# Performance work log

Measured on AMD Instinct MI355X. Metric: run time of the kernel, lower is better.

## Reference

```python
import jax, jax.numpy as jnp
import numpy as np

B, NV, NF, E = 8, 2048, 4096, 12288
DIM, DCE, DCB, K = 512, 64, 192, 128
NQ, BITS, GROUPS = 2, 14, 8


def _conv1d(x, w, b):
    # x [B, C, N], w [O, I, 3]
    y = jax.lax.conv_general_dilated(x, w, (1,), [(1, 1)], dimension_numbers=('NCH', 'OIH', 'NCH'))
    return y + b[None, :, None]


def _group_norm(x, g, b, groups=GROUPS, eps=1e-5):
    B_, C, N = x.shape
    xg = x.reshape(B_, groups, C // groups, N)
    mu = xg.mean(axis=(2, 3), keepdims=True)
    var = xg.var(axis=(2, 3), keepdims=True)
    xn = ((xg - mu) * jax.lax.rsqrt(var + eps)).reshape(B_, C, N)
    return xn * g[None, :, None] + b[None, :, None]


def _block(x, w, bias, g, beta, m):
    x = x * m
    x = _conv1d(x, w, bias)
    x = x * m
    x = _group_norm(x, g, beta)
    return jax.nn.silu(x)


def _forward(vertices, coor_embed, W_in, b_in, sage_Wl, sage_Wr, sage_b, W_cb, b_cb,
             lfq_in, lfq_out, W_out, b_out, dec_conv_w, dec_conv_b, dec_gn_g, dec_gn_b,
             W_logits, b_logits, faces, face_edges, face_edges_mask, face_mask):
    lo, hi = -1.0, 1.0
    # discretize_coors
    disc = jnp.clip(jnp.round((vertices - lo) / (hi - lo) * K - 0.5), 0, K - 1).astype(jnp.int32)
    # gather per-face vertex coords: [b, nf, 3, 3] -> [b, nf, 9]
    fc = jax.vmap(lambda v, f: v[f])(disc, faces).reshape(B, NF, 9)
    emb = coor_embed[fc].reshape(B, NF, 9 * DCE)
    x = (emb @ W_in + b_in).reshape(B * NF, DIM)
    N = B * NF
    x = jnp.concatenate([x, jnp.zeros((1, DIM), x.dtype)], axis=0)  # pad node
    offset = (jnp.arange(B) * NF)[:, None, None]
    edges = jnp.where(face_edges_mask[:, None, :], face_edges + offset, N)
    edges = edges.transpose(1, 0, 2).reshape(2, -1)
    src, tgt = edges[0], edges[1]
    ones = jnp.ones(src.shape, x.dtype)
    for l in range(sage_Wl.shape[0]):  # SAGEConv, mean aggregation
        s = jax.ops.segment_sum(x[src], tgt, num_segments=N + 1)
        c = jax.ops.segment_sum(ones, tgt, num_segments=N + 1)
        x = (s / jnp.clip(c, 1.0)[:, None]) @ sage_Wl[l] + x @ sage_Wr[l] + sage_b[l]
    x = x[:-1].reshape(B, NF, DIM)
    # quantize path: scatter-mean face-corner embeddings onto vertices
    fe = (x @ W_cb + b_cb).reshape(B, NF * 3, DCB)
    faces_m = jnp.where(face_mask[:, :, None], faces, NV).reshape(B, NF * 3).astype(jnp.int32)
    num = jax.vmap(lambda e, i: jax.ops.segment_sum(e, i, num_segments=NV + 1))(fe, faces_m)
    den = jax.vmap(lambda i: jax.ops.segment_sum(jnp.ones((NF * 3,), fe.dtype), i, num_segments=NV + 1))(faces_m)
    avg = num / jnp.clip(den, 1e-5)[..., None]
    # residual lookup-free quantization with straight-through
    res, quant = avg, jnp.zeros_like(avg)
    for q in range(NQ):
        h = res @ lfq_in[q]
        bits = jnp.where(h > 0, 1.0, -1.0).astype(h.dtype)
        bits = h + jax.lax.stop_gradient(bits - h)
        outq = bits @ lfq_out[q]
        quant = quant + outq
        res = res - outq
    # gather quantized vertex codes back to faces
    feo = jax.vmap(lambda qv, i: qv[i])(quant, faces_m).reshape(B, NF, 3 * DCB)
    feo = feo @ W_out + b_out
    # conv resnet decoder
    xd = feo.transpose(0, 2, 1)  # [b, dim, nf]
    m = face_mask[:, None, :].astype(xd.dtype)
    for blk in range(dec_conv_w.shape[0]):
        h0 = xd
        for sub in range(2):
            h0 = _block(h0, dec_conv_w[blk, sub], dec_conv_b[blk, sub], dec_gn_g[blk, sub], dec_gn_b[blk, sub], m)
        xd = h0 + xd
    dec = xd.transpose(0, 2, 1)
    return (dec @ W_logits + b_logits).reshape(B, NF, 9, K)


def setup_inputs():
    key = jax.random.key(0)
    ks = jax.random.split(key, 24)
    r = lambda i, shape, s=0.02: jax.random.normal(ks[i], shape, jnp.float32) * s
    return dict(
        vertices=jax.random.uniform(ks[0], (B, NV, 3), jnp.float32, -0.95, 0.95),
        faces=jax.random.randint(ks[1], (B, NF, 3), 0, NV),
        face_edges=jax.random.randint(ks[2], (B, 2, E), 0, NF),
        face_edges_mask=jnp.ones((B, E), bool),
        face_mask=jnp.ones((B, NF), bool),
        coor_embed=r(3, (K, DCE), 1.0),
        W_in=r(4, (9 * DCE, DIM)), b_in=r(5, (DIM,)),
        sage_Wl=r(6, (2, DIM, DIM)), sage_Wr=r(7, (2, DIM, DIM)), sage_b=r(8, (2, DIM)),
        W_cb=r(9, (DIM, 3 * DCB)), b_cb=r(10, (3 * DCB,)),
        lfq_in=r(11, (NQ, DCB, BITS), 0.05), lfq_out=r(12, (NQ, BITS, DCB), 0.05),
        W_out=r(13, (3 * DCB, DIM)), b_out=r(14, (DIM,)),
        dec_conv_w=r(15, (2, 2, DIM, DIM, 3)), dec_conv_b=r(16, (2, 2, DIM)),
        dec_gn_g=jnp.ones((2, 2, DIM), jnp.float32), dec_gn_b=jnp.zeros((2, 2, DIM), jnp.float32),
        W_logits=r(17, (DIM, 9 * K)), b_logits=r(18, (9 * K,)),
    )


def reference(vertices, faces, face_edges, face_edges_mask, face_mask, coor_embed, W_in, b_in,
              sage_Wl, sage_Wr, sage_b, W_cb, b_cb, lfq_in, lfq_out, W_out, b_out,
              dec_conv_w, dec_conv_b, dec_gn_g, dec_gn_b, W_logits, b_logits):
    return _forward(vertices, coor_embed, W_in, b_in, sage_Wl, sage_Wr, sage_b, W_cb, b_cb,
                    lfq_in, lfq_out, W_out, b_out, dec_conv_w, dec_conv_b, dec_gn_g, dec_gn_b,
                    W_logits, b_logits, faces, face_edges, face_edges_mask, face_mask)
```

## Files before the change

kernel.cpp:

```cpp
#include <hip/hip_runtime.h>
#include <hip/hip_bf16.h>
#include <cstdint>
#include <cstddef>

constexpr int BB    = 8;
constexpr int NV    = 2048;
constexpr int NF    = 4096;
constexpr int NE    = 12288;
constexpr int DIM   = 512;
constexpr int DCB   = 192;
constexpr int NQv   = 2;
constexpr int BITSv = 14;
constexpr int NFACE = BB * NF;
constexpr int NEDGE = BB * NE;
constexpr int NVB   = BB * NV;
constexpr int NFP   = NF + 2;

typedef __attribute__((ext_vector_type(8))) short bf16x8;
typedef __attribute__((ext_vector_type(4))) float f32x4;

static __device__ __forceinline__ float b2f(unsigned short u) {
    union { unsigned u; float f; } x; x.u = ((unsigned)u) << 16; return x.f;
}
static __device__ __forceinline__ unsigned short f2bu(float v) {
    __hip_bfloat16 h = __float2bfloat16(v);
    return __builtin_bit_cast(unsigned short, h);
}
static __device__ __forceinline__ void split3(float v, unsigned short& a, unsigned short& b,
                                              unsigned short& c) {
    a = f2bu(v);            float r  = v - b2f(a);
    b = f2bu(r);            float r2 = r - b2f(b);
    c = f2bu(r2);
}
static __device__ __forceinline__ void load16(const void* g, void* l) {
    __builtin_amdgcn_global_load_lds((const __attribute__((address_space(1))) unsigned int*)g,
                                     (__attribute__((address_space(3))) unsigned int*)l, 16, 0, 0);
}

static __device__ __forceinline__ void xcd_swizzle(int& bx, int& by)
{
    const int nx  = (int)gridDim.x;
    const int lin = (int)(blockIdx.x + gridDim.x * blockIdx.y);
    const int xcd = lin & 7;
    const int j   = lin >> 3;
    bx = j % nx;
    by = xcd * 32 + j / nx;
}

__global__ void k_codes(const float* __restrict__ vertices, const int* __restrict__ faces,
                        int* __restrict__ fc)
{
    const int idx = blockIdx.x * 256 + threadIdx.x;
    if (idx >= NFACE * 9) return;
    const int r = idx / 9, p = idx - r * 9;
    const int i = p / 3, j = p - i * 3;
    const int b = r >> 12;
    const int v = faces[r * 3 + i];
    const float coord = vertices[((size_t)b * NV + v) * 3 + j];
    float t = rintf((coord + 1.0f) * 0.5f * 128.0f - 0.5f);
    t = fminf(fmaxf(t, 0.0f), 127.0f);
    fc[r * 12 + p] = (int)t;
}

__global__ __launch_bounds__(256)
void k_build_T(const float* __restrict__ ce, const float* __restrict__ W_in, float* __restrict__ T)
{
    const int p = blockIdx.x;
    const int c = blockIdx.y;
    const int o = threadIdx.x * 2;
    float s0 = 0.f, s1 = 0.f;
    for (int d = 0; d < 64; ++d) {
        const float e = ce[c * 64 + d];
        const float* wr_ = W_in + (size_t)(p * 64 + d) * 512 + o;
        s0 = fmaf(e, wr_[0], s0);
        s1 = fmaf(e, wr_[1], s1);
    }
    float* dst = T + ((size_t)p * 128 + c) * 512 + o;
    dst[0] = s0; dst[1] = s1;
}

__global__ __launch_bounds__(256)
void k_xin(const int* __restrict__ fc, const float* __restrict__ T,
           const float* __restrict__ b_in,
           unsigned short* __restrict__ x0, unsigned short* __restrict__ x1,
           unsigned short* __restrict__ x2)
{
    const int r = blockIdx.x;
    const int o = threadIdx.x * 2;
    float s0 = b_in[o], s1 = b_in[o + 1];
#pragma unroll
    for (int p = 0; p < 9; ++p) {
        const int c = fc[r * 12 + p];
        const float* t = T + ((size_t)p * 128 + c) * 512 + o;
        s0 += t[0]; s1 += t[1];
    }
    unsigned short h0, m0, l0, h1, m1, l1;
    split3(s0, h0, m0, l0); split3(s1, h1, m1, l1);
    const size_t ob = (size_t)r * 512 + o;
    ushort2 u;
    u.x = h0; u.y = h1; *(ushort2*)&x0[ob] = u;
    u.x = m0; u.y = m1; *(ushort2*)&x1[ob] = u;
    u.x = l0; u.y = l1; *(ushort2*)&x2[ob] = u;
}

__global__ void k_count_e(const int* __restrict__ fe, int* __restrict__ deg)
{
    const int e = blockIdx.x * 256 + threadIdx.x;
    if (e >= NEDGE) return;
    const int b = e / NE, ee = e - b * NE;
    atomicAdd(&deg[fe[(b * 2 + 1) * NE + ee] + b * NF], 1);
}
__global__ void k_fill_e(const int* __restrict__ fe, int* __restrict__ cursor, int* __restrict__ srcE)
{
    const int e = blockIdx.x * 256 + threadIdx.x;
    if (e >= NEDGE) return;
    const int b = e / NE, ee = e - b * NE;
    const int src = fe[(b * 2 + 0) * NE + ee] + b * NF;
    const int tgt = fe[(b * 2 + 1) * NE + ee] + b * NF;
    srcE[atomicAdd(&cursor[tgt], 1)] = src;
}
__global__ void k_count_v(const int* __restrict__ faces, int* __restrict__ deg)
{
    const int q = blockIdx.x * 256 + threadIdx.x;
    if (q >= NEDGE) return;
    atomicAdd(&deg[(q / (NF * 3)) * NV + faces[q]], 1);
}
__global__ void k_fill_v(const int* __restrict__ faces, int* __restrict__ cursor, int* __restrict__ cid)
{
    const int q = blockIdx.x * 256 + threadIdx.x;
    if (q >= NEDGE) return;
    const int b = q / (NF * 3);
    cid[atomicAdd(&cursor[b * NV + faces[q]], 1)] = q;
}
__global__ void k_scan(const int* __restrict__ deg, int* __restrict__ rowstart,
                       int* __restrict__ cursor, int n)
{
    __shared__ int part[256];
    const int t = threadIdx.x;
    const int chunk = n / 256;
    int s = 0;
    for (int i = 0; i < chunk; ++i) s += deg[t * chunk + i];
    part[t] = s;
    __syncthreads();
    for (int o = 1; o < 256; o <<= 1) {
        int v = (t >= o) ? part[t - o] : 0;
        __syncthreads();
        part[t] += v;
        __syncthreads();
    }
    int base = (t == 0) ? 0 : part[t - 1];
    for (int i = 0; i < chunk; ++i) {
        const int idx = t * chunk + i;
        const int d = deg[idx];
        rowstart[idx] = base;
        cursor[idx]   = base;
        base += d;
    }
    if (t == 255) rowstart[n] = base;
}

__global__ void k_agg_e3(const unsigned short* __restrict__ p0, const unsigned short* __restrict__ p1,
                         const unsigned short* __restrict__ p2, const int* __restrict__ rowstart,
                         const int* __restrict__ srcE,
                         unsigned short* __restrict__ o0, unsigned short* __restrict__ o1,
                         unsigned short* __restrict__ o2)
{
    const int t = threadIdx.x;
    const int r = blockIdx.x * 2 + (t >> 7);
    const int c4 = (t & 127) << 2;
    const int s = rowstart[r], e = rowstart[r + 1];
    float a0 = 0.f, a1 = 0.f, a2 = 0.f, a3 = 0.f;
    for (int i = s; i < e; ++i) {
        const size_t ba = (size_t)srcE[i] * 512 + c4;
        const ushort4 u0 = *(const ushort4*)(p0 + ba);
        const ushort4 u1 = *(const ushort4*)(p1 + ba);
        const ushort4 u2 = *(const ushort4*)(p2 + ba);
        a0 += b2f(u0.x) + b2f(u1.x) + b2f(u2.x);
        a1 += b2f(u0.y) + b2f(u1.y) + b2f(u2.y);
        a2 += b2f(u0.z) + b2f(u1.z) + b2f(u2.z);
        a3 += b2f(u0.w) + b2f(u1.w) + b2f(u2.w);
    }
    const float inv = 1.0f / fmaxf((float)(e - s), 1.0f);
    a0 *= inv; a1 *= inv; a2 *= inv; a3 *= inv;
    ushort4 q0, q1, q2;
    split3(a0, q0.x, q1.x, q2.x); split3(a1, q0.y, q1.y, q2.y);
    split3(a2, q0.z, q1.z, q2.z); split3(a3, q0.w, q1.w, q2.w);
    const size_t ob = (size_t)r * 512 + c4;
    *(ushort4*)(o0 + ob) = q0; *(ushort4*)(o1 + ob) = q1; *(ushort4*)(o2 + ob) = q2;
}

__global__ void k_agg_verts(const float* __restrict__ fe, const int* __restrict__ rowstart,
                            const int* __restrict__ cid, float* __restrict__ avg)
{
    const int r = blockIdx.x;
    const int c = threadIdx.x;
    const int s = rowstart[r], e = rowstart[r + 1];
    float a = 0.f;
    for (int i = s; i < e; ++i) {
        const int q = cid[i];
        const int face = q / 3, corner = q - face * 3;
        a += fe[(size_t)face * 576 + corner * 192 + c];
    }
    avg[(size_t)r * 192 + c] = a / fmaxf((float)(e - s), 1e-5f);
}

__global__ void k_lfq(const float* __restrict__ avg, const float* __restrict__ lfq_in,
                      const float* __restrict__ lfq_out, float* __restrict__ quant)
{
    __shared__ float res[DCB];
    __shared__ float qacc[DCB];
    __shared__ float bits[BITSv];
    const int r = blockIdx.x;
    const int t = threadIdx.x;
    for (int c = t; c < DCB; c += 64) {
        res[c]  = avg[(size_t)r * DCB + c];
        qacc[c] = 0.f;
    }
    __syncthreads();
    for (int q = 0; q < NQv; ++q) {
        if (t < BITSv) {
            float h = 0.f;
            const float* w = lfq_in + q * DCB * BITSv + t;
            for (int k = 0; k < DCB; ++k) h += res[k] * w[k * BITSv];
            bits[t] = (h > 0.f) ? 1.f : -1.f;
        }
        __syncthreads();
        for (int c = t; c < DCB; c += 64) {
            float o = 0.f;
            const float* w2 = lfq_out + q * BITSv * DCB + c;
#pragma unroll
            for (int j = 0; j < BITSv; ++j) o += bits[j] * w2[j * DCB];
            qacc[c] += o;
            res[c]  -= o;
        }
        __syncthreads();
    }
    for (int c = t; c < DCB; c += 64) quant[(size_t)r * DCB + c] = qacc[c];
}

__global__ void k_gather_feo(const float* __restrict__ quant, const int* __restrict__ faces,
                             unsigned short* __restrict__ feo)
{
    const long long idx = (long long)blockIdx.x * 256 + threadIdx.x;
    if (idx >= (long long)NFACE * 576) return;
    const int row = (int)(idx / 576);
    const int col = (int)(idx - (long long)row * 576);
    const int i = col / 192, c = col - i * 192;
    const int b = row >> 12;
    const int v = faces[row * 3 + i];
    feo[idx] = f2bu(quant[((size_t)b * NV + v) * 192 + c]);
}

__global__ void k_pack_plain(const float* __restrict__ src, unsigned short* __restrict__ dst,
                             int Kd, int Nd)
{
    const int idx = blockIdx.x * 256 + threadIdx.x;
    if (idx >= Kd * Nd) return;
    const int n = idx / Kd, k = idx - n * Kd;
    dst[idx] = f2bu(src[(size_t)k * Nd + n]);
}
__global__ void k_pack_conv(const float* __restrict__ w, unsigned short* __restrict__ bt)
{
    const int idx = blockIdx.x * 256 + threadIdx.x;
    if (idx >= 4 * 512 * 1536) return;
    const int ws_ = idx / (512 * 1536);
    const int rem = idx - ws_ * 512 * 1536;
    const int o = rem / 1536, k = rem - o * 1536;
    const int tap = k >> 9, i = k & 511;
    bt[idx] = f2bu(w[(((size_t)(ws_ * 512 + o)) * 512 + i) * 3 + tap]);
}
static __device__ __forceinline__ unsigned short bplane(float w, int inner)
{
    unsigned short w0, w1, w2; split3(w, w0, w1, w2);
    const int bsel = (inner == 3) ? 2 : ((inner == 1 || inner == 4) ? 1 : 0);
    return (bsel == 0) ? w0 : ((bsel == 1) ? w1 : w2);
}
__global__ void k_pack_sage3(const float* __restrict__ wl, const float* __restrict__ wr,
                             unsigned short* __restrict__ bt)
{
    const int idx = blockIdx.x * 256 + threadIdx.x;
    if (idx >= 2 * 512 * 6144) return;
    const int l = idx / (512 * 6144);
    const int rem = idx - l * 512 * 6144;
    const int n = rem / 6144, k = rem - n * 6144;
    const int seg = k >> 9, kk = k & 511;
    const int inner = (seg >= 6) ? seg - 6 : seg;
    const float* W = ((seg >= 6) ? wr : wl) + (size_t)l * 512 * 512;
    bt[idx] = bplane(W[kk * 512 + n], inner);
}
__global__ void k_pack_cb3(const float* __restrict__ w, unsigned short* __restrict__ bt)
{
    const int idx = blockIdx.x * 256 + threadIdx.x;
    if (idx >= 640 * 3072) return;
    const int n = idx / 3072, k = idx - n * 3072;
    const int seg = k >> 9, kk = k & 511;
    const float v = (n < 576) ? w[kk * 576 + n] : 0.f;
    bt[idx] = bplane(v, seg);
}

__global__ void k_zero_guards(unsigned short* __restrict__ xdp, unsigned short* __restrict__ hp)
{
    const int idx = blockIdx.x * 256 + threadIdx.x;
    if (idx >= 8192) return;
    const int b = idx >> 10, rem = idx & 1023;
    const int row = (rem >> 9) ? (NF + 1) : 0;
    const int c = rem & 511;
    const size_t o = ((size_t)b * NFP + row) * 512 + c;
    xdp[o] = 0; hp[o] = 0;
}

template <int NSEG, int OUTE>
__global__ __launch_bounds__(256)
void k_mm_enc(const unsigned short* __restrict__ g0, const unsigned short* __restrict__ g1,
              const unsigned short* __restrict__ g2, const unsigned short* __restrict__ xA0,
              const unsigned short* __restrict__ xA1, const unsigned short* __restrict__ xA2,
              const unsigned short* __restrict__ Bt, const float* __restrict__ bias,
              void* __restrict__ C0, void* __restrict__ C1, void* __restrict__ C2, int N)
{
    constexpr int K = NSEG * 512;
    constexpr int NGRP = (NSEG == 12) ? 6 : 3;
    __shared__ __align__(16) short As[128 * 32];
    __shared__ __align__(16) short Bs[3][128 * 32];

    int bx, by;
    xcd_swizzle(bx, by);
    const int t  = threadIdx.x;
    const int m0 = by * 128;
    const int n0 = bx * 128;
    const int w  = t >> 6, l = t & 63;
    const int wr = w >> 1, wc = w & 1;
    const int lr = l & 15, lq = l >> 4;

    f32x4 acc[4][4];
#pragma unroll
    for (int i = 0; i < 4; ++i)
#pragma unroll
        for (int j = 0; j < 4; ++j)
#pragma unroll
            for (int r = 0; r < 4; ++r) acc[i][j][r] = 0.f;

    const unsigned short* const APL[6] = {g0, g1, g2, xA0, xA1, xA2};
    constexpr int SB[7]  = {0, 3, 5, 6, 9, 11, 12};
    constexpr int SL[12] = {0, 1, 3, 2, 4, 5, 6, 7, 9, 8, 10, 11};

#pragma unroll 1
    for (int kk = 0; kk < 512; kk += 32) {
#pragma unroll
        for (int grp = 0; grp < NGRP; ++grp) {
            const unsigned short* Ab = APL[grp];
            const int ns = SB[grp + 1] - SB[grp];
#pragma unroll
            for (int half = 0; half < 2; ++half) {
                const int ch = (half << 8) + t;
                const int row = ch >> 2, kq = ch & 3;
                load16(Ab + (size_t)(m0 + row) * 512 + kk + kq * 8, &As[ch * 8]);
#pragma unroll
                for (int s = 0; s < 3; ++s) {
                    if (s < ns) {
                        const int seg = SL[SB[grp] + s];
                        load16(Bt + (size_t)(n0 + row) * K + seg * 512 + kk + kq * 8,
                               &Bs[s][ch * 8]);
                    }
                }
            }
            __syncthreads();
            bf16x8 aF[4];
#pragma unroll
            for (int i = 0; i < 4; ++i)
                aF[i] = *(const bf16x8*)&As[(wr * 64 + i * 16 + lr) * 32 + lq * 8];
#pragma unroll
            for (int s = 0; s < 3; ++s) {
                if (s < ns) {
                    bf16x8 bF[4];
#pragma unroll
                    for (int j = 0; j < 4; ++j)
                        bF[j] = *(const bf16x8*)&Bs[s][(wc * 64 + j * 16 + lr) * 32 + lq * 8];
#pragma unroll
                    for (int i = 0; i < 4; ++i)
#pragma unroll
                        for (int j = 0; j < 4; ++j)
                            acc[i][j] = __builtin_amdgcn_mfma_f32_16x16x32_bf16(aF[i], bF[j],
                                                                                acc[i][j], 0, 0, 0);
                }
            }
            __syncthreads();
        }
    }

#pragma unroll
    for (int i = 0; i < 4; ++i) {
#pragma unroll
        for (int r = 0; r < 4; ++r) {
            const int m = m0 + wr * 64 + i * 16 + lq * 4 + r;
#pragma unroll
            for (int j = 0; j < 4; ++j) {
                const int n = n0 + wc * 64 + j * 16 + lr;
                if (OUTE == 0) {
                    const float v = acc[i][j][r] + bias[n];
                    unsigned short u0, u1, u2; split3(v, u0, u1, u2);
                    const size_t ob = (size_t)m * 512 + n;
                    ((unsigned short*)C0)[ob] = u0;
                    ((unsigned short*)C1)[ob] = u1;
                    ((unsigned short*)C2)[ob] = u2;
                } else {
                    if (n < N) ((float*)C0)[(size_t)m * N + n] = acc[i][j][r] + bias[n];
                }
            }
        }
    }
}

template <int AMODE, int OUT>
__global__ __launch_bounds__(256)
void k_mm(const unsigned short* __restrict__ a0, const unsigned short* __restrict__ Bt,
          const float* __restrict__ bias, void* __restrict__ C0, int N, int K)
{
    __shared__ __align__(16) short As[128 * 32];
    __shared__ __align__(16) short Bs[128 * 32];

    int bx, by;
    xcd_swizzle(bx, by);
    const int t  = threadIdx.x;
    const int m0 = by * 128;
    const int n0 = bx * 128;
    const int w  = t >> 6, l = t & 63;
    const int wr = w >> 1, wc = w & 1;
    const int lr = l & 15, lq = l >> 4;

    f32x4 acc[4][4];
#pragma unroll
    for (int i = 0; i < 4; ++i)
#pragma unroll
        for (int j = 0; j < 4; ++j)
#pragma unroll
            for (int r = 0; r < 4; ++r) acc[i][j][r] = 0.f;

    for (int k0 = 0; k0 < K; k0 += 32) {
#pragma unroll
        for (int half = 0; half < 2; ++half) {
            const int ch = (half << 8) + t;
            const int row = ch >> 2, kq = ch & 3;
            const int m = m0 + row;
            const unsigned short* ga;
            if (AMODE == 0) {
                ga = a0 + (size_t)m * K + k0 + kq * 8;
            } else if (AMODE == 1) {
                ga = a0 + (((size_t)(m + ((m >> 12) << 1) + 1)) << 9) + k0 + kq * 8;
            } else {
                const int tap = k0 >> 9;
                ga = a0 + (((size_t)(m + ((m >> 12) << 1) + tap)) << 9) + (k0 & 511) + kq * 8;
            }
            load16(ga, &As[ch * 8]);
            load16(Bt + (size_t)(n0 + row) * K + k0 + kq * 8, &Bs[ch * 8]);
        }
        __syncthreads();

        bf16x8 aF[4], bF[4];
#pragma unroll
        for (int i = 0; i < 4; ++i) {
            aF[i] = *(const bf16x8*)&As[(wr * 64 + i * 16 + lr) * 32 + lq * 8];
            bF[i] = *(const bf16x8*)&Bs[(wc * 64 + i * 16 + lr) * 32 + lq * 8];
        }
#pragma unroll
        for (int i = 0; i < 4; ++i)
#pragma unroll
            for (int j = 0; j < 4; ++j)
                acc[i][j] = __builtin_amdgcn_mfma_f32_16x16x32_bf16(aF[i], bF[j], acc[i][j], 0, 0, 0);
        __syncthreads();
    }

#pragma unroll
    for (int i = 0; i < 4; ++i) {
#pragma unroll
        for (int r = 0; r < 4; ++r) {
            const int m = m0 + wr * 64 + i * 16 + lq * 4 + r;
#pragma unroll
            for (int j = 0; j < 4; ++j) {
                const int n = n0 + wc * 64 + j * 16 + lr;
                const float bv = (OUT == 1) ? ((n < N) ? bias[n] : 0.f) : bias[n];
                const float v = acc[i][j][r] + bv;
                if (OUT == 0) {
                    ((unsigned short*)C0)[(size_t)m * 512 + n] = f2bu(v);
                } else if (OUT == 1) {
                    if (n < N) ((float*)C0)[(size_t)m * N + n] = v;
                } else {
                    ((unsigned short*)C0)[((size_t)(m + ((m >> 12) << 1) + 1)) * 512 + n] = f2bu(v);
                }
            }
        }
    }
}

__global__ __launch_bounds__(256)
void k_mm_conv(const unsigned short* __restrict__ ap, const unsigned short* __restrict__ Bt,
               const float* __restrict__ bias, unsigned short* __restrict__ C0)
{
    __shared__ __align__(16) short As[132 * 32];
    __shared__ __align__(16) short Bs[3][128 * 32];

    int bx, by;
    xcd_swizzle(bx, by);
    const int t  = threadIdx.x;
    const int m0 = by * 128;
    const int n0 = bx * 128;
    const int w  = t >> 6, l = t & 63;
    const int wr = w >> 1, wc = w & 1;
    const int lr = l & 15, lq = l >> 4;
    const int pbase = m0 + ((m0 >> 12) << 1);

    f32x4 acc[4][4];
#pragma unroll
    for (int i = 0; i < 4; ++i)
#pragma unroll
        for (int j = 0; j < 4; ++j)
#pragma unroll
            for (int r = 0; r < 4; ++r) acc[i][j][r] = 0.f;

#pragma unroll 1
    for (int kk = 0; kk < 512; kk += 32) {
#pragma unroll
        for (int rnd = 0; rnd < 2; ++rnd) {
            const int ch = (rnd << 8) + t;
            const int row = ch >> 2, kq = ch & 3;
            load16(ap + (((size_t)(pbase + row)) << 9) + kk + kq * 8, &As[ch * 8]);
        }
        if (t < 8) {
            const int ch = 512 + t;
            const int row = ch >> 2, kq = ch & 3;
            load16(ap + (((size_t)(pbase + row)) << 9) + kk + kq * 8, &As[ch * 8]);
        }
#pragma unroll
        for (int tap = 0; tap < 3; ++tap) {
#pragma unroll
            for (int half = 0; half < 2; ++half) {
                const int ch = (half << 8) + t;
                const int row = ch >> 2, kq = ch & 3;
                load16(Bt + (size_t)(n0 + row) * 1536 + tap * 512 + kk + kq * 8, &Bs[tap][ch * 8]);
            }
        }
        __syncthreads();
#pragma unroll
        for (int tap = 0; tap < 3; ++tap) {
            bf16x8 aF[4], bF[4];
#pragma unroll
            for (int i = 0; i < 4; ++i) {
                aF[i] = *(const bf16x8*)&As[(tap + wr * 64 + i * 16 + lr) * 32 + lq * 8];
                bF[i] = *(const bf16x8*)&Bs[tap][(wc * 64 + i * 16 + lr) * 32 + lq * 8];
            }
#pragma unroll
            for (int i = 0; i < 4; ++i)
#pragma unroll
                for (int j = 0; j < 4; ++j)
                    acc[i][j] = __builtin_amdgcn_mfma_f32_16x16x32_bf16(aF[i], bF[j], acc[i][j], 0, 0, 0);
        }
        __syncthreads();
    }

#pragma unroll
    for (int i = 0; i < 4; ++i) {
#pragma unroll
        for (int r = 0; r < 4; ++r) {
            const int m = m0 + wr * 64 + i * 16 + lq * 4 + r;
#pragma unroll
            for (int j = 0; j < 4; ++j) {
                const int n = n0 + wc * 64 + j * 16 + lr;
                C0[(size_t)m * 512 + n] = f2bu(acc[i][j][r] + bias[n]);
            }
        }
    }
}

__global__ __launch_bounds__(256)
void k_gn_stats(const unsigned short* __restrict__ h, float* __restrict__ stats)
{
    const int bg = blockIdx.x;
    const int b = bg >> 3, g = bg & 7;
    const int t = threadIdx.x;
    float sum = 0.f, sq = 0.f;
    const unsigned short* base = h + (size_t)b * NF * 512 + g * 64;
    for (int n = t; n < NF; n += 256) {
        const unsigned short* p = base + (size_t)n * 512;
#pragma unroll
        for (int c = 0; c < 64; c += 4) {
            const ushort4 v4 = *(const ushort4*)(p + c);
            const float f0 = b2f(v4.x), f1 = b2f(v4.y), f2 = b2f(v4.z), f3 = b2f(v4.w);
            sum += f0 + f1 + f2 + f3;
            sq  += f0 * f0 + f1 * f1 + f2 * f2 + f3 * f3;
        }
    }
    __shared__ float s1[256], s2[256];
    s1[t] = sum; s2[t] = sq;
    __syncthreads();
    for (int o = 128; o > 0; o >>= 1) {
        if (t < o) { s1[t] += s1[t + o]; s2[t] += s2[t + o]; }
        __syncthreads();
    }
    if (t == 0) {
        const float cntf = (float)(NF * 64);
        const float mean = s1[0] / cntf;
        const float var  = s2[0] / cntf - mean * mean;
        stats[bg * 2 + 0] = mean;
        stats[bg * 2 + 1] = rsqrtf(var + 1e-5f);
    }
}

__global__ void k_gn_apply(const unsigned short* __restrict__ h, const float* __restrict__ stats,
                           const float* __restrict__ gamma, const float* __restrict__ beta,
                           const unsigned short* __restrict__ resid_pad, unsigned short* __restrict__ dst_pad)
{
    const int idx = blockIdx.x * 256 + threadIdx.x;
    if (idx >= NFACE * 512 / 4) return;
    const int i4 = idx * 4;
    const int c = i4 & 511;
    const int row = i4 >> 9;
    const int b = row >> 12;
    const int g = c >> 6;
    const float mean = stats[(b * 8 + g) * 2 + 0];
    const float rstd = stats[(b * 8 + g) * 2 + 1];
    const ushort4 v4 = *(const ushort4*)(h + (size_t)row * 512 + c);
    const float4 gm = *(const float4*)&gamma[c];
    const float4 bt = *(const float4*)&beta[c];
    float o0 = (b2f(v4.x) - mean) * rstd * gm.x + bt.x;
    float o1 = (b2f(v4.y) - mean) * rstd * gm.y + bt.y;
    float o2 = (b2f(v4.z) - mean) * rstd * gm.z + bt.z;
    float o3 = (b2f(v4.w) - mean) * rstd * gm.w + bt.w;
    o0 = o0 / (1.f + expf(-o0));
    o1 = o1 / (1.f + expf(-o1));
    o2 = o2 / (1.f + expf(-o2));
    o3 = o3 / (1.f + expf(-o3));
    const size_t po = ((size_t)row + (size_t)(row >> 12) * 2 + 1) * 512 + c;
    if (resid_pad) {
        const ushort4 r4 = *(const ushort4*)(resid_pad + po);
        o0 += b2f(r4.x); o1 += b2f(r4.y); o2 += b2f(r4.z); o3 += b2f(r4.w);
    }
    ushort4 o;
    o.x = f2bu(o0); o.y = f2bu(o1); o.z = f2bu(o2); o.w = f2bu(o3);
    *(ushort4*)(dst_pad + po) = o;
}

extern "C" void kernel_launch(void* const* d_in, const int* in_sizes, int n_in,
                              void* d_out, int out_size, void* d_ws, size_t ws_size,
                              hipStream_t stream)
{
    const float* vertices   = (const float*)d_in[0];
    const int*   faces      = (const int*)  d_in[1];
    const int*   face_edges = (const int*)  d_in[2];
    const float* coor_embed = (const float*)d_in[5];
    const float* W_in    = (const float*)d_in[6];
    const float* b_in    = (const float*)d_in[7];
    const float* sage_Wl = (const float*)d_in[8];
    const float* sage_Wr = (const float*)d_in[9];
    const float* sage_b  = (const float*)d_in[10];
    const float* W_cb    = (const float*)d_in[11];
    const float* b_cb    = (const float*)d_in[12];
    const float* lfq_in  = (const float*)d_in[13];
    const float* lfq_out = (const float*)d_in[14];
    const float* W_out   = (const float*)d_in[15];
    const float* b_out   = (const float*)d_in[16];
    const float* dconv_w = (const float*)d_in[17];
    const float* dconv_b = (const float*)d_in[18];
    const float* dgn_g   = (const float*)d_in[19];
    const float* dgn_b   = (const float*)d_in[20];
    const float* W_log   = (const float*)d_in[21];
    const float* b_log   = (const float*)d_in[22];

    char* base = (char*)d_ws;
    size_t off = 0;
    auto alloc = [&](size_t bytes) { char* p = base + off; off += (bytes + 255) & ~(size_t)255; return p; };

    const size_t PLANE  = (size_t)NFACE * 512 * 2;
    char* P1 = alloc(3 * PLANE);
    char* P2 = alloc(3 * PLANE);
    char* P3 = alloc(3 * PLANE + 65536);

    unsigned short* x0 = (unsigned short*)P1;
    unsigned short* x1 = x0 + (size_t)NFACE * 512;
    unsigned short* x2 = x1 + (size_t)NFACE * 512;
    unsigned short* g0 = (unsigned short*)P2;
    unsigned short* g1 = g0 + (size_t)NFACE * 512;
    unsigned short* g2 = g1 + (size_t)NFACE * 512;
    unsigned short* y0 = (unsigned short*)P3;
    unsigned short* y1 = y0 + (size_t)NFACE * 512;
    unsigned short* y2 = y1 + (size_t)NFACE * 512;
    float*          fe   = (float*)P3;
    unsigned short* feo  = (unsigned short*)P2;
    float*          avg  = (float*)(P2 + (size_t)40 * 1024 * 1024);
    float*          quant = avg + (size_t)NVB * 192;
    unsigned short* xdp  = (unsigned short*)P3;
    unsigned short* hp   = xdp + (size_t)BB * NFP * 512;
    unsigned short* cbuf = hp + (size_t)BB * NFP * 512;

    int*   fc = (int*)  alloc((size_t)NFACE * 12 * 4);
    float* T  = (float*)alloc((size_t)9 * 128 * 512 * 4);
    unsigned short* bt_sage = (unsigned short*)alloc(2ull * 512 * 6144 * 2);
    unsigned short* bt_cb   = (unsigned short*)alloc(640ull * 3072 * 2);
    unsigned short* bt_out  = (unsigned short*)alloc(512ull * 576 * 2);
    unsigned short* bt_log  = (unsigned short*)alloc(1152ull * 512 * 2);
    unsigned short* bt_conv = (unsigned short*)alloc(4ull * 512 * 1536 * 2);
    int* degE = (int*)alloc(32768 * 4);
    int* rsE  = (int*)alloc(32772 * 4);
    int* curE = (int*)alloc(32768 * 4);
    int* srcE = (int*)alloc(98304 * 4);
    int* degV = (int*)alloc(16384 * 4);
    int* rsV  = (int*)alloc(16388 * 4);
    int* curV = (int*)alloc(16384 * 4);
    int* cidV = (int*)alloc(98304 * 4);
    float* stats = (float*)alloc(128 * 4);

    const dim3 blk(256);

    k_pack_sage3<<<dim3(24576), blk, 0, stream>>>(sage_Wl, sage_Wr, bt_sage);
    k_pack_cb3  <<<dim3(7680),  blk, 0, stream>>>(W_cb, bt_cb);
    k_pack_plain<<<dim3(1152),  blk, 0, stream>>>(W_out, bt_out, 576, 512);
    k_pack_plain<<<dim3(2304),  blk, 0, stream>>>(W_log, bt_log, 512, 1152);
    k_pack_conv <<<dim3(12288), blk, 0, stream>>>(dconv_w, bt_conv);

    hipMemsetAsync(degE, 0, 32768 * 4, stream);
    hipMemsetAsync(degV, 0, 16384 * 4, stream);
    k_count_e<<<dim3(384), blk, 0, stream>>>(face_edges, degE);
    k_count_v<<<dim3(384), blk, 0, stream>>>(faces, degV);
    k_scan<<<dim3(1), blk, 0, stream>>>(degE, rsE, curE, 32768);
    k_scan<<<dim3(1), blk, 0, stream>>>(degV, rsV, curV, 16384);
    k_fill_e<<<dim3(384), blk, 0, stream>>>(face_edges, curE, srcE);
    k_fill_v<<<dim3(384), blk, 0, stream>>>(faces, curV, cidV);

    k_codes<<<dim3(1152), blk, 0, stream>>>(vertices, faces, fc);
    k_build_T<<<dim3(9, 128), blk, 0, stream>>>(coor_embed, W_in, T);
    k_xin<<<dim3(NFACE), blk, 0, stream>>>(fc, T, b_in, x0, x1, x2);

    k_agg_e3<<<dim3(16384), blk, 0, stream>>>(x0, x1, x2, rsE, srcE, g0, g1, g2);
    k_mm_enc<12, 0><<<dim3(4, 256), blk, 0, stream>>>(g0, g1, g2, x0, x1, x2,
        bt_sage, sage_b, y0, y1, y2, 512);

    k_agg_e3<<<dim3(16384), blk, 0, stream>>>(y0, y1, y2, rsE, srcE, g0, g1, g2);
    k_mm_enc<12, 0><<<dim3(4, 256), blk, 0, stream>>>(g0, g1, g2, y0, y1, y2,
        bt_sage + (size_t)512 * 6144, sage_b + 512, x0, x1, x2, 512);

    k_mm_enc<6, 1><<<dim3(5, 256), blk, 0, stream>>>(x0, x1, x2, nullptr, nullptr, nullptr,
        bt_cb, b_cb, fe, nullptr, nullptr, 576);

    k_agg_verts<<<dim3(NVB), dim3(192), 0, stream>>>(fe, rsV, cidV, avg);
    k_lfq<<<dim3(NVB), dim3(64), 0, stream>>>(avg, lfq_in, lfq_out, quant);
    k_gather_feo<<<dim3(73728), blk, 0, stream>>>(quant, faces, feo);

    k_zero_guards<<<dim3(32), blk, 0, stream>>>(xdp, hp);
    k_mm<0, 2><<<dim3(4, 256), blk, 0, stream>>>(feo, bt_out, b_out, xdp, 512, 576);

    for (int blkI = 0; blkI < 2; ++blkI) {
        k_mm_conv<<<dim3(4, 256), blk, 0, stream>>>(xdp,
            bt_conv + (size_t)(blkI * 2 + 0) * 512 * 1536, dconv_b + (blkI * 2 + 0) * 512, cbuf);
        k_gn_stats<<<dim3(64), blk, 0, stream>>>(cbuf, stats);
        k_gn_apply<<<dim3(16384), blk, 0, stream>>>(cbuf, stats,
            dgn_g + (blkI * 2 + 0) * 512, dgn_b + (blkI * 2 + 0) * 512, nullptr, hp);
        k_mm_conv<<<dim3(4, 256), blk, 0, stream>>>(hp,
            bt_conv + (size_t)(blkI * 2 + 1) * 512 * 1536, dconv_b + (blkI * 2 + 1) * 512, cbuf);
        k_gn_stats<<<dim3(64), blk, 0, stream>>>(cbuf, stats);
        k_gn_apply<<<dim3(16384), blk, 0, stream>>>(cbuf, stats,
            dgn_g + (blkI * 2 + 1) * 512, dgn_b + (blkI * 2 + 1) * 512, xdp, xdp);
    }

    k_mm<1, 1><<<dim3(9, 256), blk, 0, stream>>>(xdp, bt_log, b_log, (float*)d_out, 1152, 512);
}
```

Measured before the change: 1.838 ms.

## Fuse face gather into output GEMM and GroupNorm stats into conv epilogue

Replaces the per-element face-corner gather kernel with a small bf16 cast of the vertex quant table, and a new GEMM kernel that gathers A rows through face indices staged in shared memory. This removes the materialized 576-wide feo buffer. The separate GroupNorm statistics kernel is removed: the conv GEMM epilogue reduces sum and sum-of-squares per block and atomically adds them into zeroed stats buffers, one per conv, and mean/rstd are computed in the apply kernel. The weight pack kernels now compute split3 once per weight and write all planes. The trade-off is float atomics, which make the order nondeterministic, and a one-pass E[x²]-mean² variance that is less numerically stable.

Result: faster. 1.754 ms (-4.5%).

```diff
diff --git a/kernel.cpp b/kernel.cpp
--- a/kernel.cpp
+++ b/kernel.cpp
@@ -238,17 +238,14 @@
     for (int c = t; c < DCB; c += 64) quant[(size_t)r * DCB + c] = qacc[c];
 }
 
-__global__ void k_gather_feo(const float* __restrict__ quant, const int* __restrict__ faces,
-                             unsigned short* __restrict__ feo)
-{
-    const long long idx = (long long)blockIdx.x * 256 + threadIdx.x;
-    if (idx >= (long long)NFACE * 576) return;
-    const int row = (int)(idx / 576);
-    const int col = (int)(idx - (long long)row * 576);
-    const int i = col / 192, c = col - i * 192;
-    const int b = row >> 12;
-    const int v = faces[row * 3 + i];
-    feo[idx] = f2bu(quant[((size_t)b * NV + v) * 192 + c]);
+__global__ void k_quant_cast(const float* __restrict__ q, unsigned short* __restrict__ qb)
+{
+    const int idx = blockIdx.x * 256 + threadIdx.x;
+    if (idx >= NVB * 48) return;
+    const float4 v = *(const float4*)(q + (size_t)idx * 4);
+    ushort4 o;
+    o.x = f2bu(v.x); o.y = f2bu(v.y); o.z = f2bu(v.z); o.w = f2bu(v.w);
+    *(ushort4*)(qb + (size_t)idx * 4) = o;
 }
 
 __global__ void k_pack_plain(const float* __restrict__ src, unsigned short* __restrict__ dst,
@@ -269,33 +266,35 @@
     const int tap = k >> 9, i = k & 511;
     bt[idx] = f2bu(w[(((size_t)(ws_ * 512 + o)) * 512 + i) * 3 + tap]);
 }
-static __device__ __forceinline__ unsigned short bplane(float w, int inner)
-{
-    unsigned short w0, w1, w2; split3(w, w0, w1, w2);
-    const int bsel = (inner == 3) ? 2 : ((inner == 1 || inner == 4) ? 1 : 0);
-    return (bsel == 0) ? w0 : ((bsel == 1) ? w1 : w2);
-}
 __global__ void k_pack_sage3(const float* __restrict__ wl, const float* __restrict__ wr,
                              unsigned short* __restrict__ bt)
 {
     const int idx = blockIdx.x * 256 + threadIdx.x;
-    if (idx >= 2 * 512 * 6144) return;
-    const int l = idx / (512 * 6144);
-    const int rem = idx - l * 512 * 6144;
-    const int n = rem / 6144, k = rem - n * 6144;
-    const int seg = k >> 9, kk = k & 511;
-    const int inner = (seg >= 6) ? seg - 6 : seg;
-    const float* W = ((seg >= 6) ? wr : wl) + (size_t)l * 512 * 512;
-    bt[idx] = bplane(W[kk * 512 + n], inner);
+    if (idx >= 2 * 2 * 512 * 512) return;
+    const int l = idx >> 19;
+    const int rem = idx & ((1 << 19) - 1);
+    const int which = rem >> 18;
+    const int r2 = rem & ((1 << 18) - 1);
+    const int n = r2 >> 9, kk = r2 & 511;
+    const float* W = (which ? wr : wl) + (size_t)l * 512 * 512;
+    unsigned short w0, w1, w2;
+    split3(W[kk * 512 + n], w0, w1, w2);
+    unsigned short* dst = bt + ((size_t)l * 512 + n) * 6144 + which * 3072 + kk;
+    dst[0 * 512] = w0; dst[2 * 512] = w0; dst[5 * 512] = w0;
+    dst[1 * 512] = w1; dst[4 * 512] = w1;
+    dst[3 * 512] = w2;
 }
 __global__ void k_pack_cb3(const float* __restrict__ w, unsigned short* __restrict__ bt)
 {
     const int idx = blockIdx.x * 256 + threadIdx.x;
-    if (idx >= 640 * 3072) return;
-    const int n = idx / 3072, k = idx - n * 3072;
-    const int seg = k >> 9, kk = k & 511;
-    const float v = (n < 576) ? w[kk * 576 + n] : 0.f;
-    bt[idx] = bplane(v, seg);
+    if (idx >= 640 * 512) return;
+    const int n = idx >> 9, kk = idx & 511;
+    unsigned short w0 = 0, w1 = 0, w2 = 0;
+    if (n < 576) split3(w[kk * 576 + n], w0, w1, w2);
+    unsigned short* dst = bt + (size_t)n * 3072 + kk;
+    dst[0 * 512] = w0; dst[2 * 512] = w0; dst[5 * 512] = w0;
+    dst[1 * 512] = w1; dst[4 * 512] = w1;
+    dst[3 * 512] = w2;
 }
 
 __global__ void k_zero_guards(unsigned short* __restrict__ xdp, unsigned short* __restrict__ hp)
@@ -444,11 +443,8 @@
             const unsigned short* ga;
             if (AMODE == 0) {
                 ga = a0 + (size_t)m * K + k0 + kq * 8;
-            } else if (AMODE == 1) {
+            } else {
                 ga = a0 + (((size_t)(m + ((m >> 12) << 1) + 1)) << 9) + k0 + kq * 8;
-            } else {
-                const int tap = k0 >> 9;
-                ga = a0 + (((size_t)(m + ((m >> 12) << 1) + tap)) << 9) + (k0 & 511) + kq * 8;
             }
             load16(ga, &As[ch * 8]);
             load16(Bt + (size_t)(n0 + row) * K + k0 + kq * 8, &Bs[ch * 8]);
@@ -479,9 +475,7 @@
                 const int n = n0 + wc * 64 + j * 16 + lr;
                 const float bv = (OUT == 1) ? ((n < N) ? bias[n] : 0.f) : bias[n];
                 const float v = acc[i][j][r] + bv;
-                if (OUT == 0) {
-                    ((unsigned short*)C0)[(size_t)m * 512 + n] = f2bu(v);
-                } else if (OUT == 1) {
+                if (OUT == 1) {
                     if (n < N) ((float*)C0)[(size_t)m * N + n] = v;
                 } else {
                     ((unsigned short*)C0)[((size_t)(m + ((m >> 12) << 1) + 1)) * 512 + n] = f2bu(v);
@@ -492,8 +486,82 @@
 }
 
 __global__ __launch_bounds__(256)
+void k_mm_out(const unsigned short* __restrict__ qb, const int* __restrict__ faces,
+              const unsigned short* __restrict__ Bt, const float* __restrict__ bias,
+              unsigned short* __restrict__ C0)
+{
+    __shared__ __align__(16) short As[128 * 32];
+    __shared__ __align__(16) short Bs[128 * 32];
+    __shared__ int fid[384];
+
+    int bx, by;
+    xcd_swizzle(bx, by);
+    const int t  = threadIdx.x;
+    const int m0 = by * 128;
+    const int n0 = bx * 128;
+    const int w  = t >> 6, l = t & 63;
+    const int wr = w >> 1, wc = w & 1;
+    const int lr = l & 15, lq = l >> 4;
+    const int vb = (m0 >> 12) << 11;
+
+    for (int i = t; i < 384; i += 256)
+        fid[i] = faces[(size_t)(m0 + i / 3) * 3 + i % 3] + vb;
+
+    f32x4 acc[4][4];
+#pragma unroll
+    for (int i = 0; i < 4; ++i)
+#pragma unroll
+        for (int j = 0; j < 4; ++j)
+#pragma unroll
+            for (int r = 0; r < 4; ++r) acc[i][j][r] = 0.f;
+
+    __syncthreads();
+
+    for (int k0 = 0; k0 < 576; k0 += 32) {
+        const int corner = k0 / 192;
+        const int cb0 = k0 - corner * 192;
+#pragma unroll
+        for (int half = 0; half < 2; ++half) {
+            const int ch = (half << 8) + t;
+            const int row = ch >> 2, kq = ch & 3;
+            const int v = fid[row * 3 + corner];
+            load16(qb + (size_t)v * 192 + cb0 + kq * 8, &As[ch * 8]);
+            load16(Bt + (size_t)(n0 + row) * 576 + k0 + kq * 8, &Bs[ch * 8]);
+        }
+        __syncthreads();
+
+        bf16x8 aF[4], bF[4];
+#pragma unroll
+        for (int i = 0; i < 4; ++i) {
+            aF[i] = *(const bf16x8*)&As[(wr * 64 + i * 16 + lr) * 32 + lq * 8];
+            bF[i] = *(const bf16x8*)&Bs[(wc * 64 + i * 16 + lr) * 32 + lq * 8];
+        }
+#pragma unroll
+        for (int i = 0; i < 4; ++i)
+#pragma unroll
+            for (int j = 0; j < 4; ++j)
+                acc[i][j] = __builtin_amdgcn_mfma_f32_16x16x32_bf16(aF[i], bF[j], acc[i][j], 0, 0, 0);
+        __syncthreads();
+    }
+
+#pragma unroll
+    for (int i = 0; i < 4; ++i) {
+#pragma unroll
+        for (int r = 0; r < 4; ++r) {
+            const int m = m0 + wr * 64 + i * 16 + lq * 4 + r;
+#pragma unroll
+            for (int j = 0; j < 4; ++j) {
+                const int n = n0 + wc * 64 + j * 16 + lr;
+                C0[((size_t)(m + ((m >> 12) << 1) + 1)) * 512 + n] = f2bu(acc[i][j][r] + bias[n]);
+            }
+        }
+    }
+}
+
+__global__ __launch_bounds__(256)
 void k_mm_conv(const unsigned short* __restrict__ ap, const unsigned short* __restrict__ Bt,
-               const float* __restrict__ bias, unsigned short* __restrict__ C0)
+               const float* __restrict__ bias, unsigned short* __restrict__ C0,
+               float* __restrict__ stats)
 {
     __shared__ __align__(16) short As[132 * 32];
     __shared__ __align__(16) short Bs[3][128 * 32];
@@ -556,6 +624,7 @@
         __syncthreads();
     }
 
+    float s1 = 0.f, s2 = 0.f;
 #pragma unroll
     for (int i = 0; i < 4; ++i) {
 #pragma unroll
@@ -564,43 +633,27 @@
 #pragma unroll
             for (int j = 0; j < 4; ++j) {
                 const int n = n0 + wc * 64 + j * 16 + lr;
-                C0[(size_t)m * 512 + n] = f2bu(acc[i][j][r] + bias[n]);
+                const float v = acc[i][j][r] + bias[n];
+                C0[(size_t)m * 512 + n] = f2bu(v);
+                s1 += v; s2 += v * v;
             }
         }
     }
-}
-
-__global__ __launch_bounds__(256)
-void k_gn_stats(const unsigned short* __restrict__ h, float* __restrict__ stats)
-{
-    const int bg = blockIdx.x;
-    const int b = bg >> 3, g = bg & 7;
-    const int t = threadIdx.x;
-    float sum = 0.f, sq = 0.f;
-    const unsigned short* base = h + (size_t)b * NF * 512 + g * 64;
-    for (int n = t; n < NF; n += 256) {
-        const unsigned short* p = base + (size_t)n * 512;
-#pragma unroll
-        for (int c = 0; c < 64; c += 4) {
-            const ushort4 v4 = *(const ushort4*)(p + c);
-            const float f0 = b2f(v4.x), f1 = b2f(v4.y), f2 = b2f(v4.z), f3 = b2f(v4.w);
-            sum += f0 + f1 + f2 + f3;
-            sq  += f0 * f0 + f1 * f1 + f2 * f2 + f3 * f3;
-        }
-    }
-    __shared__ float s1[256], s2[256];
-    s1[t] = sum; s2[t] = sq;
+
+    float* red = (float*)As;
+    red[t] = s1; red[t + 256] = s2;
     __syncthreads();
-    for (int o = 128; o > 0; o >>= 1) {
-        if (t < o) { s1[t] += s1[t + o]; s2[t] += s2[t + o]; }
-        __syncthreads();
-    }
-    if (t == 0) {
-        const float cntf = (float)(NF * 64);
-        const float mean = s1[0] / cntf;
-        const float var  = s2[0] / cntf - mean * mean;
-        stats[bg * 2 + 0] = mean;
-        stats[bg * 2 + 1] = rsqrtf(var + 1e-5f);
+    if (t < 128) { red[t] += red[t + 128]; red[t + 256] += red[t + 384]; }
+    __syncthreads();
+    for (int o = 32; o > 0; o >>= 1) {
+        if (t < 128 && (t & 63) < o) { red[t] += red[t + o]; red[t + 256] += red[t + 256 + o]; }
+        __syncthreads();
+    }
+    if (t == 0 || t == 64) {
+        const int b = m0 >> 12;
+        const int g = (n0 >> 6) + (t >> 6);
+        atomicAdd(&stats[(b * 8 + g) * 2 + 0], red[t]);
+        atomicAdd(&stats[(b * 8 + g) * 2 + 1], red[t + 256]);
     }
 }
 
@@ -615,8 +668,11 @@
     const int row = i4 >> 9;
     const int b = row >> 12;
     const int g = c >> 6;
-    const float mean = stats[(b * 8 + g) * 2 + 0];
-    const float rstd = stats[(b * 8 + g) * 2 + 1];
+    const float cnt = (float)(NF * 64);
+    const float S1 = stats[(b * 8 + g) * 2 + 0];
+    const float S2 = stats[(b * 8 + g) * 2 + 1];
+    const float mean = S1 / cnt;
+    const float rstd = rsqrtf(S2 / cnt - mean * mean + 1e-5f);
     const ushort4 v4 = *(const ushort4*)(h + (size_t)row * 512 + c);
     const float4 gm = *(const float4*)&gamma[c];
     const float4 bt = *(const float4*)&beta[c];
@@ -683,7 +739,7 @@
     unsigned short* y1 = y0 + (size_t)NFACE * 512;
     unsigned short* y2 = y1 + (size_t)NFACE * 512;
     float*          fe   = (float*)P3;
-    unsigned short* feo  = (unsigned short*)P2;
+    unsigned short* qb   = (unsigned short*)P2;
     float*          avg  = (float*)(P2 + (size_t)40 * 1024 * 1024);
     float*          quant = avg + (size_t)NVB * 192;
     unsigned short* xdp  = (unsigned short*)P3;
@@ -705,18 +761,19 @@
     int* rsV  = (int*)alloc(16388 * 4);
     int* curV = (int*)alloc(16384 * 4);
     int* cidV = (int*)alloc(98304 * 4);
-    float* stats = (float*)alloc(128 * 4);
+    float* stats = (float*)alloc(4 * 128 * 4);
 
     const dim3 blk(256);
 
-    k_pack_sage3<<<dim3(24576), blk, 0, stream>>>(sage_Wl, sage_Wr, bt_sage);
-    k_pack_cb3  <<<dim3(7680),  blk, 0, stream>>>(W_cb, bt_cb);
-    k_pack_plain<<<dim3(1152),  blk, 0, stream>>>(W_out, bt_out, 576, 512);
-    k_pack_plain<<<dim3(2304),  blk, 0, stream>>>(W_log, bt_log, 512, 1152);
+    k_pack_sage3<<<dim3(4096), blk, 0, stream>>>(sage_Wl, sage_Wr, bt_sage);
+    k_pack_cb3  <<<dim3(1280), blk, 0, stream>>>(W_cb, bt_cb);
+    k_pack_plain<<<dim3(1152), blk, 0, stream>>>(W_out, bt_out, 576, 512);
+    k_pack_plain<<<dim3(2304), blk, 0, stream>>>(W_log, bt_log, 512, 1152);
     k_pack_conv <<<dim3(12288), blk, 0, stream>>>(dconv_w, bt_conv);
 
     hipMemsetAsync(degE, 0, 32768 * 4, stream);
     hipMemsetAsync(degV, 0, 16384 * 4, stream);
+    hipMemsetAsync(stats, 0, 4 * 128 * 4, stream);
     k_count_e<<<dim3(384), blk, 0, stream>>>(face_edges, degE);
     k_count_v<<<dim3(384), blk, 0, stream>>>(faces, degV);
     k_scan<<<dim3(1), blk, 0, stream>>>(degE, rsE, curE, 32768);
@@ -741,21 +798,21 @@
 
     k_agg_verts<<<dim3(NVB), dim3(192), 0, stream>>>(fe, rsV, cidV, avg);
     k_lfq<<<dim3(NVB), dim3(64), 0, stream>>>(avg, lfq_in, lfq_out, quant);
-    k_gather_feo<<<dim3(73728), blk, 0, stream>>>(quant, faces, feo);
+    k_quant_cast<<<dim3(3072), blk, 0, stream>>>(quant, qb);
 
     k_zero_guards<<<dim3(32), blk, 0, stream>>>(xdp, hp);
-    k_mm<0, 2><<<dim3(4, 256), blk, 0, stream>>>(feo, bt_out, b_out, xdp, 512, 576);
+    k_mm_out<<<dim3(4, 256), blk, 0, stream>>>(qb, faces, bt_out, b_out, xdp);
 
     for (int blkI = 0; blkI < 2; ++blkI) {
         k_mm_conv<<<dim3(4, 256), blk, 0, stream>>>(xdp,
-            bt_conv + (size_t)(blkI * 2 + 0) * 512 * 1536, dconv_b + (blkI * 2 + 0) * 512, cbuf);
-        k_gn_stats<<<dim3(64), blk, 0, stream>>>(cbuf, stats);
-        k_gn_apply<<<dim3(16384), blk, 0, stream>>>(cbuf, stats,
+            bt_conv + (size_t)(blkI * 2 + 0) * 512 * 1536, dconv_b + (blkI * 2 + 0) * 512,
+            cbuf, stats + (blkI * 2 + 0) * 128);
+        k_gn_apply<<<dim3(16384), blk, 0, stream>>>(cbuf, stats + (blkI * 2 + 0) * 128,
             dgn_g + (blkI * 2 + 0) * 512, dgn_b + (blkI * 2 + 0) * 512, nullptr, hp);
         k_mm_conv<<<dim3(4, 256), blk, 0, stream>>>(hp,
-            bt_conv + (size_t)(blkI * 2 + 1) * 512 * 1536, dconv_b + (blkI * 2 + 1) * 512, cbuf);
-        k_gn_stats<<<dim3(64), blk, 0, stream>>>(cbuf, stats);
-        k_gn_apply<<<dim3(16384), blk, 0, stream>>>(cbuf, stats,
+            bt_conv + (size_t)(blkI * 2 + 1) * 512 * 1536, dconv_b + (blkI * 2 + 1) * 512,
+            cbuf, stats + (blkI * 2 + 1) * 128);
+        k_gn_apply<<<dim3(16384), blk, 0, stream>>>(cbuf, stats + (blkI * 2 + 1) * 128,
             dgn_g + (blkI * 2 + 1) * 512, dgn_b + (blkI * 2 + 1) * 512, xdp, xdp);
     }
 
```
